# Kernel tuning notes

Measured on AMD Instinct MI355X. Metric: run time of the kernel, lower is better.

Reference implementation:

```python
import jax, jax.numpy as jnp
import numpy as np

N_HEAD, D_K, D_V, D_MODEL, D_O = 8, 64, 64, 512, 512
B, S = 2, 4096

def setup_inputs() -> dict:
    key = jax.random.key(0)
    ks = jax.random.split(key, 11)
    s = 1.0 / np.sqrt(D_MODEL)
    so = 1.0 / np.sqrt(N_HEAD * D_V)
    return {
        'q': jax.random.normal(ks[0], (B, S, D_MODEL), jnp.float32),
        'k': jax.random.normal(ks[1], (B, S, D_MODEL), jnp.float32),
        'v': jax.random.normal(ks[2], (B, S, D_MODEL), jnp.float32),
        'Wq': jax.random.uniform(ks[3], (D_MODEL, N_HEAD * D_K), jnp.float32, -s, s),
        'bq': jax.random.uniform(ks[4], (N_HEAD * D_K,), jnp.float32, -s, s),
        'Wk': jax.random.uniform(ks[5], (D_MODEL, N_HEAD * D_K), jnp.float32, -s, s),
        'bk': jax.random.uniform(ks[6], (N_HEAD * D_K,), jnp.float32, -s, s),
        'Wv': jax.random.uniform(ks[7], (D_MODEL, N_HEAD * D_V), jnp.float32, -s, s),
        'bv': jax.random.uniform(ks[8], (N_HEAD * D_V,), jnp.float32, -s, s),
        'Wo': jax.random.uniform(ks[9], (N_HEAD * D_V, D_O), jnp.float32, -so, so),
        'bo': jax.random.uniform(ks[10], (D_O,), jnp.float32, -so, so),
    }

def reference(q, k, v, Wq, bq, Wk, bk, Wv, bv, Wo, bo):
    b, nq, _ = q.shape
    nk = k.shape[1]
    scale = jnp.asarray(np.power(D_K, 0.5), q.dtype)
    # project and split heads: [b, s, h, d]
    qh = (q @ Wq + bq).reshape(b, nq, N_HEAD, D_K)
    kh = (k @ Wk + bk).reshape(b, nk, N_HEAD, D_K)
    vh = (v @ Wv + bv).reshape(b, nk, N_HEAD, D_V)
    # scaled dot-product attention (full score matrix, as in original)
    scores = jnp.einsum('bqhd,bkhd->bhqk', qh, kh) / scale
    attn = jax.nn.softmax(scores, axis=-1)
    out = jnp.einsum('bhqk,bkhd->bqhd', attn, vh)
    # concat heads (head-major over d_v, matching the original view) and output proj
    out = out.reshape(b, nq, N_HEAD * D_V)
    return out @ Wo + bo
```

## Files before the change

### kernel.cpp

```cpp
#include <hip/hip_runtime.h>
#include <hip/hip_bf16.h>

#define NHEAD 8
#define DK_ 64
#define DM_ 512
#define S_LEN 4096
#define NTOK 8192

typedef __bf16 bf16x8 __attribute__((ext_vector_type(8)));
typedef float f32x4 __attribute__((ext_vector_type(4)));
typedef float f32x16 __attribute__((ext_vector_type(16)));
typedef unsigned int uint4v __attribute__((ext_vector_type(4)));

__device__ __forceinline__ unsigned short f2bf(float f) {
    union { float f; unsigned u; } x; x.f = f;
    unsigned u = x.u;
    u += 0x7FFFu + ((u >> 16) & 1u);
    return (unsigned short)(u >> 16);
}

#if __has_builtin(__builtin_amdgcn_cvt_pk_bf16_f32)
__device__ __forceinline__ unsigned int pkbf(float a, float b) {
    auto r = __builtin_amdgcn_cvt_pk_bf16_f32(a, b);
    unsigned int u; __builtin_memcpy(&u, &r, 4); return u;
}
#else
__device__ __forceinline__ unsigned int pkbf(float a, float b) {
    return (unsigned)f2bf(a) | ((unsigned)f2bf(b) << 16);
}
#endif

#if __has_builtin(__builtin_amdgcn_exp2f)
#define EXP2F(x) __builtin_amdgcn_exp2f(x)
#else
#define EXP2F(x) exp2f(x)
#endif

#if __has_builtin(__builtin_amdgcn_permlane32_swap)
__device__ __forceinline__ void pl32swap(unsigned int& a, unsigned int& b) {
    auto r = __builtin_amdgcn_permlane32_swap(a, b, false, false);
    a = r[0]; b = r[1];
}
#else
__device__ __forceinline__ void pl32swap(unsigned int& a, unsigned int& b) {
    int lane = threadIdx.x & 63;
    unsigned int ax = __shfl_xor((int)a, 32, 64);
    unsigned int bx = __shfl_xor((int)b, 32, 64);
    unsigned int na = (lane < 32) ? a : bx;
    unsigned int nb = (lane < 32) ? ax : b;
    a = na; b = nb;
}
#endif

#define GLOAD_LDS16(gptr, ldsbase) \
    __builtin_amdgcn_global_load_lds((const __attribute__((address_space(1))) unsigned int*)(gptr), \
                                     (__attribute__((address_space(3))) unsigned int*)(ldsbase), 16, 0, 0)

__global__ __launch_bounds__(256) void xcvt(const float* __restrict__ q, const float* __restrict__ k,
                                            const float* __restrict__ v, unsigned short* __restrict__ Xbf) {
    int z = blockIdx.y;
    const float* X = (z == 0) ? q : (z == 1) ? k : v;
    size_t off = (size_t)blockIdx.x * 1024 + threadIdx.x * 4;
    float4 val = *(const float4*)&X[off];
    uint2 o; o.x = pkbf(val.x, val.y); o.y = pkbf(val.z, val.w);
    *(uint2*)&Xbf[(size_t)z * NTOK * DM_ + off] = o;
}

__global__ __launch_bounds__(256) void wtrans(const float* __restrict__ Wq, const float* __restrict__ Wk,
                                              const float* __restrict__ Wv, const float* __restrict__ Wo,
                                              unsigned short* __restrict__ Wt) {
    int z = blockIdx.z;
    const float* W = (z == 0) ? Wq : (z == 1) ? Wk : (z == 2) ? Wv : Wo;
    unsigned short* out = Wt + (size_t)z * DM_ * DM_;
    __shared__ float t[64][65];
    int bn = blockIdx.x * 64, bk = blockIdx.y * 64;
    int tid = threadIdx.x;
    int r0 = tid >> 4, c4 = (tid & 15) * 4;
#pragma unroll
    for (int i = 0; i < 4; i++) {
        int r = r0 + i * 16;
        float4 v = *(const float4*)&W[(size_t)(bk + r) * DM_ + bn + c4];
        t[r][c4] = v.x; t[r][c4 + 1] = v.y; t[r][c4 + 2] = v.z; t[r][c4 + 3] = v.w;
    }
    __syncthreads();
    int n0 = tid >> 4, k4 = (tid & 15) * 4;
#pragma unroll
    for (int i = 0; i < 4; i++) {
        int n = n0 + i * 16;
        ushort4 o;
        o.x = f2bf(t[k4 + 0][n]); o.y = f2bf(t[k4 + 1][n]);
        o.z = f2bf(t[k4 + 2][n]); o.w = f2bf(t[k4 + 3][n]);
        *(ushort4*)&out[(size_t)(bn + n) * DM_ + bk + k4] = o;
    }
}

__device__ __forceinline__ void proj_epilogue(int z, f32x4 (&acc)[4][4], const float* bias,
                                              unsigned short* out, float scale,
                                              int m0, int n0, int mb, int nb, int ln, int qd) {
    float bvv[4];
#pragma unroll
    for (int nt = 0; nt < 4; nt++) bvv[nt] = bias[n0 + nb + nt * 16 + ln];
#pragma unroll
    for (int mt = 0; mt < 4; mt++) {
        int mrow0 = m0 + mb + mt * 16 + qd * 4;
        int b = mrow0 >> 12, s = mrow0 & 4095;
#pragma unroll
        for (int nt = 0; nt < 4; nt++) {
            int ncol = n0 + nb + nt * 16 + ln;
            int h = ncol >> 6, d = ncol & 63;
            if (z == 2) {
                uint2 o;
                o.x = pkbf((acc[mt][nt][0] + bvv[nt]) * scale, (acc[mt][nt][1] + bvv[nt]) * scale);
                o.y = pkbf((acc[mt][nt][2] + bvv[nt]) * scale, (acc[mt][nt][3] + bvv[nt]) * scale);
                *(uint2*)&out[((size_t)(b * NHEAD + h) * DK_ + d) * S_LEN + s] = o;
            } else {
#pragma unroll
                for (int r = 0; r < 4; r++)
                    out[((size_t)(b * NHEAD + h) * S_LEN + (s + r)) * DK_ + d] =
                        f2bf((acc[mt][nt][r] + bvv[nt]) * scale);
            }
        }
    }
}

__global__ __launch_bounds__(256, 3) void qkv_bf(const unsigned short* __restrict__ Xbf,
                                                 const unsigned short* __restrict__ Wt,
                                                 const float* __restrict__ bq, const float* __restrict__ bk,
                                                 const float* __restrict__ bv,
                                                 unsigned short* __restrict__ Qh, unsigned short* __restrict__ Kh,
                                                 unsigned short* __restrict__ VhT) {
    int z = blockIdx.z;
    const unsigned short* X = Xbf + (size_t)z * NTOK * DM_;
    const unsigned short* W = Wt + (size_t)z * DM_ * DM_;
    const float* bias = (z == 0) ? bq : (z == 1) ? bk : bv;
    unsigned short* out = (z == 0) ? Qh : (z == 1) ? Kh : VhT;
    float scale = (z == 0) ? 0.125f * 1.44269504f : 1.0f;

    __shared__ unsigned short As[128 * 40];
    __shared__ unsigned short Bs[128 * 40];
    int tid = threadIdx.x;
    int n0 = blockIdx.x * 128, m0 = blockIdx.y * 128;
    int w = tid >> 6, lane = tid & 63;
    int ln = lane & 15, qd = lane >> 4;
    int mb = (w >> 1) * 64, nb = (w & 1) * 64;

    f32x4 acc[4][4];
#pragma unroll
    for (int i = 0; i < 4; i++)
#pragma unroll
        for (int j = 0; j < 4; j++) { f32x4 zz = {0.f, 0.f, 0.f, 0.f}; acc[i][j] = zz; }

    for (int kk = 0; kk < DM_; kk += 32) {
        __syncthreads();
#pragma unroll
        for (int i = 0; i < 2; i++) {
            int idx = i * 256 + tid;
            int row = idx >> 2, k8 = (idx & 3) * 8;
            uint4 va = *(const uint4*)&X[(size_t)(m0 + row) * DM_ + kk + k8];
            *(uint4*)&As[row * 40 + k8] = va;
            uint4 vb = *(const uint4*)&W[(size_t)(n0 + row) * DM_ + kk + k8];
            *(uint4*)&Bs[row * 40 + k8] = vb;
        }
        __syncthreads();
        bf16x8 af[4], bf[4];
#pragma unroll
        for (int mt = 0; mt < 4; mt++) af[mt] = *(const bf16x8*)&As[(mb + mt * 16 + ln) * 40 + qd * 8];
#pragma unroll
        for (int nt = 0; nt < 4; nt++) bf[nt] = *(const bf16x8*)&Bs[(nb + nt * 16 + ln) * 40 + qd * 8];
#pragma unroll
        for (int mt = 0; mt < 4; mt++)
#pragma unroll
            for (int nt = 0; nt < 4; nt++)
                acc[mt][nt] = __builtin_amdgcn_mfma_f32_16x16x32_bf16(af[mt], bf[nt], acc[mt][nt], 0, 0, 0);
    }
    proj_epilogue(z, acc, bias, out, scale, m0, n0, mb, nb, ln, qd);
}

__global__ __launch_bounds__(256, 3) void qkv_proj(const float* __restrict__ xq, const float* __restrict__ xk,
                                                   const float* __restrict__ xv, const unsigned short* __restrict__ Wt,
                                                   const float* __restrict__ bq, const float* __restrict__ bk,
                                                   const float* __restrict__ bv,
                                                   unsigned short* __restrict__ Qh, unsigned short* __restrict__ Kh,
                                                   unsigned short* __restrict__ VhT) {
    int z = blockIdx.z;
    const float* X = (z == 0) ? xq : (z == 1) ? xk : xv;
    const unsigned short* W = Wt + (size_t)z * DM_ * DM_;
    const float* bias = (z == 0) ? bq : (z == 1) ? bk : bv;
    unsigned short* out = (z == 0) ? Qh : (z == 1) ? Kh : VhT;
    float scale = (z == 0) ? 0.125f * 1.44269504f : 1.0f;

    __shared__ unsigned short As[128 * 40];
    __shared__ unsigned short Bs[128 * 40];
    int tid = threadIdx.x;
    int n0 = blockIdx.x * 128, m0 = blockIdx.y * 128;
    int w = tid >> 6, lane = tid & 63;
    int ln = lane & 15, qd = lane >> 4;
    int mb = (w >> 1) * 64, nb = (w & 1) * 64;

    f32x4 acc[4][4];
#pragma unroll
    for (int i = 0; i < 4; i++)
#pragma unroll
        for (int j = 0; j < 4; j++) { f32x4 zz = {0.f, 0.f, 0.f, 0.f}; acc[i][j] = zz; }

    for (int kk = 0; kk < DM_; kk += 32) {
        __syncthreads();
#pragma unroll
        for (int i = 0; i < 4; i++) {
            int idx = i * 256 + tid;
            int row = idx >> 3, k4 = (idx & 7) * 4;
            float4 v = *(const float4*)&X[(size_t)(m0 + row) * DM_ + kk + k4];
            uint2 o; o.x = pkbf(v.x, v.y); o.y = pkbf(v.z, v.w);
            *(uint2*)&As[row * 40 + k4] = o;
        }
#pragma unroll
        for (int i = 0; i < 2; i++) {
            int idx = i * 256 + tid;
            int row = idx >> 2, k8 = (idx & 3) * 8;
            uint4 v = *(const uint4*)&W[(size_t)(n0 + row) * DM_ + kk + k8];
            *(uint4*)&Bs[row * 40 + k8] = v;
        }
        __syncthreads();
        bf16x8 af[4], bf[4];
#pragma unroll
        for (int mt = 0; mt < 4; mt++) af[mt] = *(const bf16x8*)&As[(mb + mt * 16 + ln) * 40 + qd * 8];
#pragma unroll
        for (int nt = 0; nt < 4; nt++) bf[nt] = *(const bf16x8*)&Bs[(nb + nt * 16 + ln) * 40 + qd * 8];
#pragma unroll
        for (int mt = 0; mt < 4; mt++)
#pragma unroll
            for (int nt = 0; nt < 4; nt++)
                acc[mt][nt] = __builtin_amdgcn_mfma_f32_16x16x32_bf16(af[mt], bf[nt], acc[mt][nt], 0, 0, 0);
    }
    proj_epilogue(z, acc, bias, out, scale, m0, n0, mb, nb, ln, qd);
}

__global__ __launch_bounds__(256, 2) void flash_attn(const unsigned short* __restrict__ Qh,
                                                     const unsigned short* __restrict__ Kh,
                                                     const unsigned short* __restrict__ VhT,
                                                     unsigned short* __restrict__ Ao) {
    __shared__ unsigned short Ks[2][64 * 64];
    __shared__ unsigned short Vs[2][64 * 64];
    int i = blockIdx.x;
    int bh = (i & 7) + 8 * ((i >> 3) & 1);
    int qb = i >> 4;
    int tid = threadIdx.x;
    int w = tid >> 6, lane = tid & 63;
    int ln = lane & 31, hf = lane >> 5;
    int swz = ln & 7;
    int q0 = qb * 128 + w * 32;
    const unsigned short* Qp = Qh + (size_t)bh * S_LEN * DK_;
    const unsigned short* Kp = Kh + (size_t)bh * S_LEN * DK_;
    const unsigned short* Vp = VhT + (size_t)bh * DK_ * S_LEN;

    int sr = lane >> 3;
    int sc = (lane & 7) ^ sr;
    const unsigned short* ksrc = Kp + (size_t)(w * 16 + sr) * DK_ + sc * 8;
    const unsigned short* vsrc = Vp + (size_t)(w * 16 + sr) * S_LEN + sc * 8;

    bf16x8 qf[4];
#pragma unroll
    for (int s = 0; s < 4; s++)
        qf[s] = *(const bf16x8*)&Qp[(size_t)(q0 + ln) * DK_ + s * 16 + hf * 8];

    f32x16 oacc[2];
    { f32x16 z = {0.f}; oacc[0] = z; oacc[1] = z; }
    float lsum = 0.f;

    GLOAD_LDS16(ksrc, &Ks[0][w * 1024]);
    GLOAD_LDS16(ksrc + (size_t)8 * DK_, &Ks[0][w * 1024 + 512]);
    GLOAD_LDS16(vsrc, &Vs[0][w * 1024]);
    GLOAD_LDS16(vsrc + (size_t)8 * S_LEN, &Vs[0][w * 1024 + 512]);

    int p = 0;
    for (int ks = 0; ks < S_LEN; ks += 64, p ^= 1) {
        __syncthreads();
        if (ks + 64 < S_LEN) {
            const unsigned short* kn = ksrc + (size_t)(ks + 64) * DK_;
            const unsigned short* vn = vsrc + (ks + 64);
            GLOAD_LDS16(kn, &Ks[p ^ 1][w * 1024]);
            GLOAD_LDS16(kn + (size_t)8 * DK_, &Ks[p ^ 1][w * 1024 + 512]);
            GLOAD_LDS16(vn, &Vs[p ^ 1][w * 1024]);
            GLOAD_LDS16(vn + (size_t)8 * S_LEN, &Vs[p ^ 1][w * 1024 + 512]);
        }
        const unsigned short* KsT = &Ks[p][0];
        const unsigned short* VsT = &Vs[p][0];

#pragma unroll
        for (int kb = 0; kb < 2; kb++) {
            f32x16 st = {0.f};
#pragma unroll
            for (int s = 0; s < 4; s++) {
                bf16x8 kf = *(const bf16x8*)&KsT[(kb * 32 + ln) * 64 + ((2 * s + hf) ^ swz) * 8];
                st = __builtin_amdgcn_mfma_f32_32x32x16_bf16(kf, qf[s], st, 0, 0, 0);
            }
            float e[16];
#pragma unroll
            for (int r = 0; r < 16; r++) e[r] = EXP2F(st[r]);
            lsum += ((e[0] + e[1]) + (e[2] + e[3])) + ((e[4] + e[5]) + (e[6] + e[7]))
                  + ((e[8] + e[9]) + (e[10] + e[11])) + ((e[12] + e[13]) + (e[14] + e[15]));
            unsigned int g[8];
#pragma unroll
            for (int gi = 0; gi < 8; gi++) g[gi] = pkbf(e[2 * gi], e[2 * gi + 1]);
            pl32swap(g[0], g[2]); pl32swap(g[1], g[3]);
            pl32swap(g[4], g[6]); pl32swap(g[5], g[7]);
            bf16x8 b0, b1;
            { uint4v t = {g[0], g[1], g[2], g[3]}; __builtin_memcpy(&b0, &t, 16); }
            { uint4v t = {g[4], g[5], g[6], g[7]}; __builtin_memcpy(&b1, &t, 16); }
#pragma unroll
            for (int dt = 0; dt < 2; dt++) {
                int s0 = kb * 2;
                bf16x8 vf0 = *(const bf16x8*)&VsT[(dt * 32 + ln) * 64 + ((2 * s0 + hf) ^ swz) * 8];
                bf16x8 vf1 = *(const bf16x8*)&VsT[(dt * 32 + ln) * 64 + ((2 * s0 + 2 + hf) ^ swz) * 8];
                oacc[dt] = __builtin_amdgcn_mfma_f32_32x32x16_bf16(vf0, b0, oacc[dt], 0, 0, 0);
                oacc[dt] = __builtin_amdgcn_mfma_f32_32x32x16_bf16(vf1, b1, oacc[dt], 0, 0, 0);
            }
        }
    }

    float ltot = lsum + __shfl_xor(lsum, 32, 64);
    float inv = 1.0f / ltot;

    int bb = bh >> 3, hh = bh & 7;
    int token = bb * S_LEN + q0 + ln;
#pragma unroll
    for (int dt = 0; dt < 2; dt++)
#pragma unroll
        for (int gi = 0; gi < 8; gi++) {
            int d = dt * 32 + 2 * (gi & 1) + 8 * (gi >> 1) + 4 * hf;
            unsigned int o = pkbf(oacc[dt][2 * gi] * inv, oacc[dt][2 * gi + 1] * inv);
            *(unsigned int*)&Ao[(size_t)token * DM_ + hh * DK_ + d] = o;
        }
}

__global__ __launch_bounds__(256) void out_gemm(const unsigned short* __restrict__ A,
                                                const unsigned short* __restrict__ Wt,
                                                const float* __restrict__ bias, float* __restrict__ out) {
    __shared__ unsigned short As[128 * 40];
    __shared__ unsigned short Bs[128 * 40];
    int tid = threadIdx.x;
    int n0 = blockIdx.x * 128, m0 = blockIdx.y * 128;
    int w = tid >> 6, lane = tid & 63;
    int ln = lane & 15, qd = lane >> 4;
    int mb = (w >> 1) * 64, nb = (w & 1) * 64;

    f32x4 acc[4][4];
#pragma unroll
    for (int i = 0; i < 4; i++)
#pragma unroll
        for (int j = 0; j < 4; j++) { f32x4 z = {0.f, 0.f, 0.f, 0.f}; acc[i][j] = z; }

    for (int kk = 0; kk < DM_; kk += 32) {
        __syncthreads();
#pragma unroll
        for (int i = 0; i < 2; i++) {
            int idx = i * 256 + tid;
            int row = idx >> 2, k8 = (idx & 3) * 8;
            uint4 va = *(const uint4*)&A[(size_t)(m0 + row) * DM_ + kk + k8];
            *(uint4*)&As[row * 40 + k8] = va;
            uint4 vb = *(const uint4*)&Wt[(size_t)(n0 + row) * DM_ + kk + k8];
            *(uint4*)&Bs[row * 40 + k8] = vb;
        }
        __syncthreads();
        bf16x8 af[4], bf[4];
#pragma unroll
        for (int mt = 0; mt < 4; mt++) af[mt] = *(const bf16x8*)&As[(mb + mt * 16 + ln) * 40 + qd * 8];
#pragma unroll
        for (int nt = 0; nt < 4; nt++) bf[nt] = *(const bf16x8*)&Bs[(nb + nt * 16 + ln) * 40 + qd * 8];
#pragma unroll
        for (int mt = 0; mt < 4; mt++)
#pragma unroll
            for (int nt = 0; nt < 4; nt++)
                acc[mt][nt] = __builtin_amdgcn_mfma_f32_16x16x32_bf16(af[mt], bf[nt], acc[mt][nt], 0, 0, 0);
    }

    float bv[4];
#pragma unroll
    for (int nt = 0; nt < 4; nt++) bv[nt] = bias[n0 + nb + nt * 16 + ln];
#pragma unroll
    for (int mt = 0; mt < 4; mt++) {
        int mrow0 = m0 + mb + mt * 16 + qd * 4;
#pragma unroll
        for (int nt = 0; nt < 4; nt++) {
            int ncol = n0 + nb + nt * 16 + ln;
#pragma unroll
            for (int r = 0; r < 4; r++)
                out[(size_t)(mrow0 + r) * DM_ + ncol] = acc[mt][nt][r] + bv[nt];
        }
    }
}

extern "C" void kernel_launch(void* const* d_in, const int* in_sizes, int n_in,
                              void* d_out, int out_size, void* d_ws, size_t ws_size,
                              hipStream_t stream) {
    const float* q  = (const float*)d_in[0];
    const float* k  = (const float*)d_in[1];
    const float* v  = (const float*)d_in[2];
    const float* Wq = (const float*)d_in[3];
    const float* bq = (const float*)d_in[4];
    const float* Wk = (const float*)d_in[5];
    const float* bk = (const float*)d_in[6];
    const float* Wv = (const float*)d_in[7];
    const float* bv = (const float*)d_in[8];
    const float* Wo = (const float*)d_in[9];
    const float* bo = (const float*)d_in[10];
    float* out = (float*)d_out;

    unsigned short* Wt  = (unsigned short*)d_ws;
    unsigned short* Qh  = Wt + (size_t)4 * DM_ * DM_;
    unsigned short* Kh  = Qh + (size_t)NTOK * DM_;
    unsigned short* VhT = Kh + (size_t)NTOK * DM_;
    unsigned short* tail = VhT + (size_t)NTOK * DM_;

    size_t need_bf = ((size_t)4 * DM_ * DM_ + (size_t)6 * NTOK * DM_) * 2;

    wtrans<<<dim3(8, 8, 4), 256, 0, stream>>>(Wq, Wk, Wv, Wo, Wt);
    unsigned short* Ao = tail;
    if (ws_size >= need_bf) {
        unsigned short* Xbf = tail;
        xcvt<<<dim3(4096, 3), 256, 0, stream>>>(q, k, v, Xbf);
        qkv_bf<<<dim3(4, 64, 3), 256, 0, stream>>>(Xbf, Wt, bq, bk, bv, Qh, Kh, VhT);
    } else {
        qkv_proj<<<dim3(4, 64, 3), 256, 0, stream>>>(q, k, v, Wt, bq, bk, bv, Qh, Kh, VhT);
    }
    flash_attn<<<dim3(512), 256, 0, stream>>>(Qh, Kh, VhT, Ao);
    out_gemm<<<dim3(4, 64), 256, 0, stream>>>(Ao, Wt + (size_t)3 * DM_ * DM_, bo, out);
}
```

Before: 242.4 us.

## Split flash attention over two KV halves and merge partial results

Adds a split-KV variant of the attention kernel. Each query block processes only half of the key/value sequence, which doubles the grid from 512 to 1024 blocks and raises CU occupancy. Each half writes unnormalized fp32 partial outputs and row sums, and a new merge kernel adds them, normalizes, and converts the result to bf16 for the output GEMM. The cost is extra fp32 global traffic, one more kernel launch, and a larger workspace requirement; if the workspace is too small the code falls back to the old path.

Result: no change. 242.2 us (-0.1%).

```diff
diff --git a/kernel.cpp b/kernel.cpp
--- a/kernel.cpp
+++ b/kernel.cpp
@@ -333,6 +333,130 @@
         }
 }
 
+__global__ __launch_bounds__(256, 4) void flash_attn_sp(const unsigned short* __restrict__ Qh,
+                                                        const unsigned short* __restrict__ Kh,
+                                                        const unsigned short* __restrict__ VhT,
+                                                        float* __restrict__ Opart,
+                                                        float* __restrict__ lpart) {
+    __shared__ unsigned short Ks[2][64 * 64];
+    __shared__ unsigned short Vs[2][64 * 64];
+    int i = blockIdx.x;
+    int bh = (i & 7) + 8 * ((i >> 3) & 1);
+    int qb = (i >> 4) & 31;
+    int sp = i >> 9;
+    int ks0 = sp * (S_LEN / 2);
+    int ks1 = ks0 + (S_LEN / 2);
+    int tid = threadIdx.x;
+    int w = tid >> 6, lane = tid & 63;
+    int ln = lane & 31, hf = lane >> 5;
+    int swz = ln & 7;
+    int q0 = qb * 128 + w * 32;
+    const unsigned short* Qp = Qh + (size_t)bh * S_LEN * DK_;
+    const unsigned short* Kp = Kh + (size_t)bh * S_LEN * DK_;
+    const unsigned short* Vp = VhT + (size_t)bh * DK_ * S_LEN;
+
+    int sr = lane >> 3;
+    int sc = (lane & 7) ^ sr;
+    const unsigned short* ksrc = Kp + (size_t)(w * 16 + sr) * DK_ + sc * 8;
+    const unsigned short* vsrc = Vp + (size_t)(w * 16 + sr) * S_LEN + sc * 8;
+
+    bf16x8 qf[4];
+#pragma unroll
+    for (int s = 0; s < 4; s++)
+        qf[s] = *(const bf16x8*)&Qp[(size_t)(q0 + ln) * DK_ + s * 16 + hf * 8];
+
+    f32x16 oacc[2];
+    { f32x16 z = {0.f}; oacc[0] = z; oacc[1] = z; }
+    float lsum = 0.f;
+
+    GLOAD_LDS16(ksrc + (size_t)ks0 * DK_, &Ks[0][w * 1024]);
+    GLOAD_LDS16(ksrc + (size_t)(ks0 + 8) * DK_, &Ks[0][w * 1024 + 512]);
+    GLOAD_LDS16(vsrc + ks0, &Vs[0][w * 1024]);
+    GLOAD_LDS16(vsrc + ks0 + (size_t)8 * S_LEN, &Vs[0][w * 1024 + 512]);
+
+    int p = 0;
+    for (int ks = ks0; ks < ks1; ks += 64, p ^= 1) {
+        __syncthreads();
+        if (ks + 64 < ks1) {
+            const unsigned short* kn = ksrc + (size_t)(ks + 64) * DK_;
+            const unsigned short* vn = vsrc + (ks + 64);
+            GLOAD_LDS16(kn, &Ks[p ^ 1][w * 1024]);
+            GLOAD_LDS16(kn + (size_t)8 * DK_, &Ks[p ^ 1][w * 1024 + 512]);
+            GLOAD_LDS16(vn, &Vs[p ^ 1][w * 1024]);
+            GLOAD_LDS16(vn + (size_t)8 * S_LEN, &Vs[p ^ 1][w * 1024 + 512]);
+        }
+        const unsigned short* KsT = &Ks[p][0];
+        const unsigned short* VsT = &Vs[p][0];
+
+#pragma unroll
+        for (int kb = 0; kb < 2; kb++) {
+            f32x16 st = {0.f};
+#pragma unroll
+            for (int s = 0; s < 4; s++) {
+                bf16x8 kf = *(const bf16x8*)&KsT[(kb * 32 + ln) * 64 + ((2 * s + hf) ^ swz) * 8];
+                st = __builtin_amdgcn_mfma_f32_32x32x16_bf16(kf, qf[s], st, 0, 0, 0);
+            }
+            float e[16];
+#pragma unroll
+            for (int r = 0; r < 16; r++) e[r] = EXP2F(st[r]);
+            lsum += ((e[0] + e[1]) + (e[2] + e[3])) + ((e[4] + e[5]) + (e[6] + e[7]))
+                  + ((e[8] + e[9]) + (e[10] + e[11])) + ((e[12] + e[13]) + (e[14] + e[15]));
+            unsigned int g[8];
+#pragma unroll
+            for (int gi = 0; gi < 8; gi++) g[gi] = pkbf(e[2 * gi], e[2 * gi + 1]);
+            pl32swap(g[0], g[2]); pl32swap(g[1], g[3]);
+            pl32swap(g[4], g[6]); pl32swap(g[5], g[7]);
+            bf16x8 b0, b1;
+            { uint4v t = {g[0], g[1], g[2], g[3]}; __builtin_memcpy(&b0, &t, 16); }
+            { uint4v t = {g[4], g[5], g[6], g[7]}; __builtin_memcpy(&b1, &t, 16); }
+#pragma unroll
+            for (int dt = 0; dt < 2; dt++) {
+                int s0 = kb * 2;
+                bf16x8 vf0 = *(const bf16x8*)&VsT[(dt * 32 + ln) * 64 + ((2 * s0 + hf) ^ swz) * 8];
+                bf16x8 vf1 = *(const bf16x8*)&VsT[(dt * 32 + ln) * 64 + ((2 * s0 + 2 + hf) ^ swz) * 8];
+                oacc[dt] = __builtin_amdgcn_mfma_f32_32x32x16_bf16(vf0, b0, oacc[dt], 0, 0, 0);
+                oacc[dt] = __builtin_amdgcn_mfma_f32_32x32x16_bf16(vf1, b1, oacc[dt], 0, 0, 0);
+            }
+        }
+    }
+
+    float ltot = lsum + __shfl_xor(lsum, 32, 64);
+    if (hf == 0)
+        lpart[(size_t)sp * (16 * S_LEN) + (size_t)bh * S_LEN + q0 + ln] = ltot;
+
+    int bb = bh >> 3, hh = bh & 7;
+    int token = bb * S_LEN + q0 + ln;
+    float* op = Opart + (size_t)sp * NTOK * DM_;
+#pragma unroll
+    for (int dt = 0; dt < 2; dt++)
+#pragma unroll
+        for (int gi = 0; gi < 8; gi++) {
+            int d = dt * 32 + 2 * (gi & 1) + 8 * (gi >> 1) + 4 * hf;
+            float2 o; o.x = oacc[dt][2 * gi]; o.y = oacc[dt][2 * gi + 1];
+            *(float2*)&op[(size_t)token * DM_ + hh * DK_ + d] = o;
+        }
+}
+
+__global__ __launch_bounds__(256) void merge_split(const float* __restrict__ Opart,
+                                                   const float* __restrict__ lpart,
+                                                   unsigned short* __restrict__ Ao) {
+    size_t e = ((size_t)blockIdx.x * 256 + threadIdx.x) * 4;
+    int token = (int)(e >> 9);
+    int c = (int)(e & 511);
+    int hh = c >> 6;
+    int bb = token >> 12, s = token & 4095;
+    size_t li = (size_t)(bb * NHEAD + hh) * S_LEN + s;
+    float l0 = lpart[li];
+    float l1 = lpart[(size_t)16 * S_LEN + li];
+    float inv = 1.0f / (l0 + l1);
+    float4 a = *(const float4*)&Opart[e];
+    float4 b = *(const float4*)&Opart[(size_t)NTOK * DM_ + e];
+    uint2 o;
+    o.x = pkbf((a.x + b.x) * inv, (a.y + b.y) * inv);
+    o.y = pkbf((a.z + b.z) * inv, (a.w + b.w) * inv);
+    *(uint2*)&Ao[e] = o;
+}
+
 __global__ __launch_bounds__(256) void out_gemm(const unsigned short* __restrict__ A,
                                                 const unsigned short* __restrict__ Wt,
                                                 const float* __restrict__ bias, float* __restrict__ out) {
@@ -412,17 +536,33 @@
     unsigned short* VhT = Kh + (size_t)NTOK * DM_;
     unsigned short* tail = VhT + (size_t)NTOK * DM_;
 
+    float* Opart = (float*)tail;
+    float* lpart = Opart + (size_t)2 * NTOK * DM_;
+    unsigned short* Ao_sp = (unsigned short*)(lpart + (size_t)2 * 16 * S_LEN);
+
+    size_t head_b  = ((size_t)4 * DM_ * DM_ + (size_t)3 * NTOK * DM_) * 2;
+    size_t need_sp = head_b + (size_t)2 * NTOK * DM_ * 4 + (size_t)2 * 16 * S_LEN * 4 + (size_t)NTOK * DM_ * 2;
     size_t need_bf = ((size_t)4 * DM_ * DM_ + (size_t)6 * NTOK * DM_) * 2;
 
     wtrans<<<dim3(8, 8, 4), 256, 0, stream>>>(Wq, Wk, Wv, Wo, Wt);
-    unsigned short* Ao = tail;
-    if (ws_size >= need_bf) {
+    if (ws_size >= need_sp) {
         unsigned short* Xbf = tail;
         xcvt<<<dim3(4096, 3), 256, 0, stream>>>(q, k, v, Xbf);
         qkv_bf<<<dim3(4, 64, 3), 256, 0, stream>>>(Xbf, Wt, bq, bk, bv, Qh, Kh, VhT);
+        flash_attn_sp<<<dim3(1024), 256, 0, stream>>>(Qh, Kh, VhT, Opart, lpart);
+        merge_split<<<dim3(4096), 256, 0, stream>>>(Opart, lpart, Ao_sp);
+        out_gemm<<<dim3(4, 64), 256, 0, stream>>>(Ao_sp, Wt + (size_t)3 * DM_ * DM_, bo, out);
+    } else if (ws_size >= need_bf) {
+        unsigned short* Xbf = tail;
+        unsigned short* Ao = tail;
+        xcvt<<<dim3(4096, 3), 256, 0, stream>>>(q, k, v, Xbf);
+        qkv_bf<<<dim3(4, 64, 3), 256, 0, stream>>>(Xbf, Wt, bq, bk, bv, Qh, Kh, VhT);
+        flash_attn<<<dim3(512), 256, 0, stream>>>(Qh, Kh, VhT, Ao);
+        out_gemm<<<dim3(4, 64), 256, 0, stream>>>(Ao, Wt + (size_t)3 * DM_ * DM_, bo, out);
     } else {
+        unsigned short* Ao = tail;
         qkv_proj<<<dim3(4, 64, 3), 256, 0, stream>>>(q, k, v, Wt, bq, bk, bv, Qh, Kh, VhT);
-    }
-    flash_attn<<<dim3(512), 256, 0, stream>>>(Qh, Kh, VhT, Ao);
-    out_gemm<<<dim3(4, 64), 256, 0, stream>>>(Ao, Wt + (size_t)3 * DM_ * DM_, bo, out);
-}
+        flash_attn<<<dim3(512), 256, 0, stream>>>(Qh, Kh, VhT, Ao);
+        out_gemm<<<dim3(4, 64), 256, 0, stream>>>(Ao, Wt + (size_t)3 * DM_ * DM_, bo, out);
+    }
+}
```
